# Optimization experiments

Measured on AMD Instinct MI355X. Metric: run time of the kernel, lower is better.

Reference implementation:

```python
import jax, jax.numpy as jnp
import numpy as np

N_REGS, R_BIT, N_OPS, FLIP = 8, 16, 16, 2

def bit2dec(bits):
    # little-endian soft bits -> decimal: sum_k b_k * 2^k
    k = jnp.arange(bits.shape[-1], dtype=bits.dtype)
    return jnp.sum(bits * jnp.exp2(k), axis=-1)

def addr_w(idx, n):
    # differentiable soft one-hot over n slots (linear interpolation kernel)
    grid = jnp.arange(n, dtype=idx.dtype)
    return jnp.maximum(1.0 - jnp.abs(idx[..., None] - grid), 0.0)

def setup_inputs():
    key = jax.random.key(0)
    ks = jax.random.split(key, 12)
    B, H, I, L = 8192, 512, 1024, 16
    return dict(
        z_hidden=jax.random.normal(ks[0], (B, H), jnp.float32),
        P_op=jax.random.uniform(ks[1], (B, L, 4), dtype=jnp.float32),
        P_dst=jax.random.uniform(ks[2], (B, L, 3), dtype=jnp.float32),
        P_src1=jax.random.uniform(ks[3], (B, L, 3), dtype=jnp.float32),
        P_src2=jax.random.uniform(ks[4], (B, L, 3), dtype=jnp.float32),
        P_imm=jax.random.uniform(ks[5], (B, L, 3), dtype=jnp.float32),
        Proglen=jax.random.uniform(ks[6], (B, 4), dtype=jnp.float32),
        group_num=16,
        W1=jax.random.normal(ks[7], (H, I), jnp.float32) / np.sqrt(H).astype(np.float32),
        b1=jnp.zeros((I,), jnp.float32),
        WR=jax.random.normal(ks[8], (I, N_REGS * R_BIT), jnp.float32) / np.sqrt(I).astype(np.float32),
        bR=jnp.zeros((N_REGS * R_BIT,), jnp.float32),
        Wt=jax.random.normal(ks[9], (I, 1), jnp.float32) / np.sqrt(I).astype(np.float32),
        bt=jnp.zeros((1,), jnp.float32),
        W_r2h=jax.random.normal(ks[10], (N_REGS, H), jnp.float32) / np.sqrt(N_REGS).astype(np.float32),
        b_r2h=jnp.zeros((H,), jnp.float32),
        ln_g=jnp.ones((H,), jnp.float32),
        ln_b=jnp.zeros((H,), jnp.float32),
    )

def reference(z_hidden, P_op, P_dst, P_src1, P_src2, P_imm, Proglen, group_num,
              W1, b1, WR, bR, Wt, bt, W_r2h, b_r2h, ln_g, ln_b):
    B, L, G = z_hidden.shape[0], P_op.shape[1], group_num
    # ---- Augmentation_Layer: MLP head -> R soft-bits + threshold ----
    h = jax.nn.relu(z_hidden @ W1 + b1)
    R_bits = jax.nn.sigmoid(h @ WR + bR).reshape(B, N_REGS, R_BIT)
    threshold = jax.nn.sigmoid(h @ Wt + bt)                 # [B,1]
    # ---- GroupSample.generate4R: flip FLIP random R-bits per candidate (cand 0 = original) ----
    idx = jax.random.randint(jax.random.key(42), (B, G, FLIP), 0, N_REGS * R_BIT)
    mask = jnp.clip(jax.nn.one_hot(idx, N_REGS * R_BIT, dtype=jnp.float32).sum(-2), 0.0, 1.0)
    mask = mask.at[:, 0].set(0.0).reshape(B, G, N_REGS, R_BIT)
    Rb = R_bits[:, None]                                    # [B,1,n_regs,r_bit]
    R = bit2dec(Rb + mask * (1.0 - 2.0 * Rb))               # [B,G,n_regs] decimals
    M = jnp.zeros_like(R)
    prog_len = jnp.broadcast_to(bit2dec(Proglen)[:, None], (B, G))
    dec = lambda x: bit2dec(x).T                            # [L,B]
    prog = (dec(P_op), dec(P_dst), dec(P_src1), dec(P_src2), dec(P_imm),
            jnp.arange(L, dtype=jnp.float32))

    # ---- MultiInterpreter: differentiable soft register machine ----
    def step(carry, xs):
        R, M = carry
        op_t, dst_t, s1_t, s2_t, imm_t, t = xs
        bc = lambda v: jnp.broadcast_to(v[:, None], (B, G))
        op_t, dst_t, s1_t, s2_t, imm_t = map(bc, (op_t, dst_t, s1_t, s2_t, imm_t))
        active = jnp.clip(prog_len - t, 0.0, 1.0)           # halt mask [B,G]
        w_d = addr_w(dst_t, N_REGS)                         # [B,G,n_regs]
        w_1 = addr_w(s1_t, N_REGS)
        w_2 = addr_w(s2_t, N_REGS)
        w_op = addr_w(op_t, N_OPS)                          # [B,G,16]
        r1 = jnp.sum(w_1 * R, -1); r2 = jnp.sum(w_2 * R, -1)
        m1 = jnp.sum(w_1 * M, -1); old = jnp.sum(w_d * R, -1)
        results = jnp.stack([
            old,                       # 0 NOP
            r1 + r2,                   # 1 ADD
            r1 - r2,                   # 2 SUB
            r1 * r2 / 65536.0,         # 3 MUL (scaled by 2^r_bit)
            r1,                        # 4 MOV
            imm_t,                     # 5 LOADI
            r1 + imm_t,                # 6 ADDI
            jnp.maximum(r1, r2),       # 7 MAX
            jnp.minimum(r1, r2),       # 8 MIN
            -r1,                       # 9 NEG
            0.5 * r1,                  # 10 SHR
            r2,                        # 11 MOV2
            m1,                        # 12 LOAD M[src1]
            old,                       # 13 STORE (reg unchanged)
            jnp.abs(r1),               # 14 ABS
            old,                       # 15 NOP
        ], axis=-1)
        res = jnp.sum(w_op * results, -1)                   # [B,G]
        p_store = w_op[..., 13]
        R = R + active[..., None] * w_d * (res[..., None] - R)
        M = M + (active * p_store)[..., None] * w_d * (r1[..., None] - M)
        return (R, M), None

    (R, M), _ = jax.lax.scan(step, (R, M), prog)
    # ---- register2hidden + LayerNorm ----
    reg_hidden = R @ W_r2h + b_r2h                          # [B,G,H]
    mu = reg_hidden.mean(-1, keepdims=True)
    var = reg_hidden.var(-1, keepdims=True)
    reg_hidden = (reg_hidden - mu) * jax.lax.rsqrt(var + 1e-5) * ln_g + ln_b
    return reg_hidden, threshold
```

## Files before the change

### kernel.cpp

```cpp
#include <hip/hip_runtime.h>
#include <stdint.h>

typedef __attribute__((ext_vector_type(8))) short short8;
typedef __attribute__((ext_vector_type(4))) float f32x4;
typedef __attribute__((ext_vector_type(8))) unsigned short ushort8;
typedef __attribute__((ext_vector_type(4))) unsigned short ushort4v;

__device__ __forceinline__ unsigned short f2bf(float f) {
  uint32_t u = __float_as_uint(f);
  uint32_t r = (u + 0x7fffu + ((u >> 16) & 1u)) >> 16;
  return (unsigned short)r;
}
__device__ __forceinline__ float bf2f(unsigned short v) {
  return __uint_as_float(((uint32_t)v) << 16);
}

__device__ __forceinline__ uint32_t rotl32(uint32_t v, int d) { return (v << d) | (v >> (32 - d)); }

__device__ __forceinline__ void threefry2x32(uint32_t k0, uint32_t k1, uint32_t& x0, uint32_t& x1) {
  const uint32_t ks2 = k0 ^ k1 ^ 0x1BD11BDAu;
  x0 += k0; x1 += k1;
  x0 += x1; x1 = rotl32(x1, 13); x1 ^= x0;
  x0 += x1; x1 = rotl32(x1, 15); x1 ^= x0;
  x0 += x1; x1 = rotl32(x1, 26); x1 ^= x0;
  x0 += x1; x1 = rotl32(x1, 6);  x1 ^= x0;
  x0 += k1; x1 += ks2 + 1u;
  x0 += x1; x1 = rotl32(x1, 17); x1 ^= x0;
  x0 += x1; x1 = rotl32(x1, 29); x1 ^= x0;
  x0 += x1; x1 = rotl32(x1, 16); x1 ^= x0;
  x0 += x1; x1 = rotl32(x1, 24); x1 ^= x0;
  x0 += ks2; x1 += k0 + 2u;
  x0 += x1; x1 = rotl32(x1, 13); x1 ^= x0;
  x0 += x1; x1 = rotl32(x1, 15); x1 ^= x0;
  x0 += x1; x1 = rotl32(x1, 26); x1 ^= x0;
  x0 += x1; x1 = rotl32(x1, 6);  x1 ^= x0;
  x0 += k0; x1 += k1 + 3u;
  x0 += x1; x1 = rotl32(x1, 17); x1 ^= x0;
  x0 += x1; x1 = rotl32(x1, 29); x1 ^= x0;
  x0 += x1; x1 = rotl32(x1, 16); x1 ^= x0;
  x0 += x1; x1 = rotl32(x1, 24); x1 ^= x0;
  x0 += k1; x1 += ks2 + 4u;
  x0 += x1; x1 = rotl32(x1, 13); x1 ^= x0;
  x0 += x1; x1 = rotl32(x1, 15); x1 ^= x0;
  x0 += x1; x1 = rotl32(x1, 26); x1 ^= x0;
  x0 += x1; x1 = rotl32(x1, 6);  x1 ^= x0;
  x0 += ks2; x1 += k0 + 5u;
}

__global__ __launch_bounds__(256) void cast_bf16(const float* __restrict__ in,
                                                 unsigned short* __restrict__ o, int n8) {
  const int i = blockIdx.x * 256 + threadIdx.x;
  if (i >= n8) return;
  const float4 a = reinterpret_cast<const float4*>(in)[i * 2];
  const float4 b = reinterpret_cast<const float4*>(in)[i * 2 + 1];
  ushort8 u;
  u[0] = f2bf(a.x); u[1] = f2bf(a.y); u[2] = f2bf(a.z); u[3] = f2bf(a.w);
  u[4] = f2bf(b.x); u[5] = f2bf(b.y); u[6] = f2bf(b.z); u[7] = f2bf(b.w);
  reinterpret_cast<ushort8*>(o)[i] = u;
}

__global__ __launch_bounds__(256) void transpose_cast(const float* __restrict__ W1,
                                                      const float* __restrict__ WR,
                                                      unsigned short* __restrict__ W1t,
                                                      unsigned short* __restrict__ WRt) {
  __shared__ float t[32][33];
  const int tid = threadIdx.x;
  const float* src; unsigned short* dst; int N, K, k0, n0;
  if (blockIdx.x < 512) {
    src = W1; dst = W1t; N = 1024; K = 512;
    k0 = (blockIdx.x & 15) * 32; n0 = (blockIdx.x >> 4) * 32;
  } else {
    const int b2 = blockIdx.x - 512;
    src = WR; dst = WRt; N = 128; K = 1024;
    k0 = (b2 & 31) * 32; n0 = (b2 >> 5) * 32;
  }
  {
    const int row = tid >> 3, c4 = (tid & 7) * 4;
    const float4 v = *reinterpret_cast<const float4*>(&src[(size_t)(k0 + row) * N + n0 + c4]);
    t[row][c4] = v.x; t[row][c4 + 1] = v.y; t[row][c4 + 2] = v.z; t[row][c4 + 3] = v.w;
  }
  __syncthreads();
  {
    const int n = tid >> 3, k4 = (tid & 7) * 4;
    ushort4v o;
    o.x = f2bf(t[k4 + 0][n]); o.y = f2bf(t[k4 + 1][n]);
    o.z = f2bf(t[k4 + 2][n]); o.w = f2bf(t[k4 + 3][n]);
    *reinterpret_cast<ushort4v*>(&dst[(size_t)(n0 + n) * K + k0 + k4]) = o;
  }
}

__global__ __launch_bounds__(256) void gemm_fused(const unsigned short* __restrict__ zb,
                                                  const unsigned short* __restrict__ W1t,
                                                  const float* __restrict__ b1,
                                                  const unsigned short* __restrict__ WRt,
                                                  unsigned short* __restrict__ h,
                                                  float* __restrict__ part, int B) {
  __shared__ __align__(16) char smem[34816];
  auto As = reinterpret_cast<unsigned short (*)[56]>(smem);
  auto Bs = reinterpret_cast<unsigned short (*)[56]>(smem + 14336);
  auto H2 = reinterpret_cast<unsigned short (*)[136]>(smem);

  const int tid = threadIdx.x;
  const int lane = tid & 63, wave = tid >> 6;
  const int wm = wave >> 1, wn = wave & 1;
  const int bx = blockIdx.x, bm = blockIdx.y * 128, bn = bx * 128;

  f32x4 acc[4][4];
#pragma unroll
  for (int i = 0; i < 4; ++i)
#pragma unroll
    for (int j = 0; j < 4; ++j) acc[i][j] = (f32x4)0.f;

  const int sm = tid >> 1, skh = (tid & 1) * 16;
  const int fr = lane & 15, kc = (lane >> 4) * 8;
  const int lr = (lane >> 4) * 4, lc = lane & 15;

  for (int k0 = 0; k0 < 512; k0 += 32) {
    {
      const unsigned short* ap = &zb[(size_t)(bm + sm) * 512 + k0 + skh];
      *reinterpret_cast<ushort8*>(&As[sm][skh]) = *reinterpret_cast<const ushort8*>(ap);
      *reinterpret_cast<ushort8*>(&As[sm][skh + 8]) = *reinterpret_cast<const ushort8*>(ap + 8);
    }
    {
      const unsigned short* bp = &W1t[(size_t)(bn + sm) * 512 + k0 + skh];
      *reinterpret_cast<ushort8*>(&Bs[sm][skh]) = *reinterpret_cast<const ushort8*>(bp);
      *reinterpret_cast<ushort8*>(&Bs[sm][skh + 8]) = *reinterpret_cast<const ushort8*>(bp + 8);
    }
    __syncthreads();
    short8 af[4], bfv[4];
#pragma unroll
    for (int f = 0; f < 4; ++f)
      af[f] = *reinterpret_cast<const short8*>(&As[wm * 64 + f * 16 + fr][kc]);
#pragma unroll
    for (int f = 0; f < 4; ++f)
      bfv[f] = *reinterpret_cast<const short8*>(&Bs[wn * 64 + f * 16 + fr][kc]);
#pragma unroll
    for (int fm = 0; fm < 4; ++fm)
#pragma unroll
      for (int fn = 0; fn < 4; ++fn)
        acc[fm][fn] = __builtin_amdgcn_mfma_f32_16x16x32_bf16(af[fm], bfv[fn], acc[fm][fn], 0, 0, 0);
    __syncthreads();
  }

#pragma unroll
  for (int fn = 0; fn < 4; ++fn) {
    const int col_l = wn * 64 + fn * 16 + lc;
    const float bv = b1[bn + col_l];
#pragma unroll
    for (int fm = 0; fm < 4; ++fm) {
      const int row_l0 = wm * 64 + fm * 16 + lr;
#pragma unroll
      for (int r = 0; r < 4; ++r)
        H2[row_l0 + r][col_l] = f2bf(fmaxf(acc[fm][fn][r] + bv, 0.f));
    }
  }
  __syncthreads();

  {
    const int row = tid >> 1, c0 = (tid & 1) * 64;
    unsigned short* hp = &h[(size_t)(bm + row) * 1024 + bn + c0];
#pragma unroll
    for (int j = 0; j < 8; ++j)
      *reinterpret_cast<ushort8*>(hp + j * 8) = *reinterpret_cast<const ushort8*>(&H2[row][c0 + j * 8]);
  }

  f32x4 acc2[4][4];
#pragma unroll
  for (int i = 0; i < 4; ++i)
#pragma unroll
    for (int j = 0; j < 4; ++j) acc2[i][j] = (f32x4)0.f;

#pragma unroll
  for (int ks = 0; ks < 4; ++ks) {
    short8 af2[4], bf2v[4];
#pragma unroll
    for (int fm = 0; fm < 4; ++fm)
      af2[fm] = *reinterpret_cast<const short8*>(&H2[wm * 64 + fm * 16 + fr][ks * 32 + kc]);
#pragma unroll
    for (int fn = 0; fn < 4; ++fn)
      bf2v[fn] = *reinterpret_cast<const short8*>(
          &WRt[(size_t)(wn * 64 + fn * 16 + fr) * 1024 + bn + ks * 32 + kc]);
#pragma unroll
    for (int fm = 0; fm < 4; ++fm)
#pragma unroll
      for (int fn = 0; fn < 4; ++fn)
        acc2[fm][fn] = __builtin_amdgcn_mfma_f32_16x16x32_bf16(af2[fm], bf2v[fn], acc2[fm][fn], 0, 0, 0);
  }

  float* pp = part + (size_t)bx * B * 128;
#pragma unroll
  for (int fn = 0; fn < 4; ++fn) {
    const int col = wn * 64 + fn * 16 + lc;
#pragma unroll
    for (int fm = 0; fm < 4; ++fm) {
      const int row0 = bm + wm * 64 + fm * 16 + lr;
#pragma unroll
      for (int r = 0; r < 4; ++r)
        pp[(size_t)(row0 + r) * 128 + col] = acc2[fm][fn][r];
    }
  }
}

__global__ __launch_bounds__(256) void reduce_sig(const float* __restrict__ part,
                                                  const float* __restrict__ bR,
                                                  float* __restrict__ out, int total4) {
  const int i = blockIdx.x * 256 + threadIdx.x;
  if (i >= total4) return;
  const float4* p = reinterpret_cast<const float4*>(part);
  float4 s = p[i];
#pragma unroll
  for (int j = 1; j < 8; ++j) {
    const float4 q = p[i + (size_t)j * total4];
    s.x += q.x; s.y += q.y; s.z += q.z; s.w += q.w;
  }
  const int col = (i * 4) & 127;
  const float4 bb = *reinterpret_cast<const float4*>(&bR[col]);
  float4 o;
  o.x = 1.f / (1.f + expf(-(s.x + bb.x)));
  o.y = 1.f / (1.f + expf(-(s.y + bb.y)));
  o.z = 1.f / (1.f + expf(-(s.z + bb.z)));
  o.w = 1.f / (1.f + expf(-(s.w + bb.w)));
  reinterpret_cast<float4*>(out)[i] = o;
}

__global__ __launch_bounds__(256) void thresh_kernel(const unsigned short* __restrict__ h,
                                                     const float* __restrict__ Wt,
                                                     const float* __restrict__ bt,
                                                     float* __restrict__ out, int B) {
  const int lane = threadIdx.x & 63;
  const int row = blockIdx.x * 4 + (threadIdx.x >> 6);
  if (row >= B) return;
  const unsigned short* hr = h + (size_t)row * 1024;
  float s = 0.f;
#pragma unroll
  for (int it = 0; it < 2; ++it) {
    const int k = (lane + it * 64) * 8;
    const ushort8 a = *reinterpret_cast<const ushort8*>(&hr[k]);
    const float4 w0 = *reinterpret_cast<const float4*>(&Wt[k]);
    const float4 w1 = *reinterpret_cast<const float4*>(&Wt[k + 4]);
    s += bf2f(a[0]) * w0.x + bf2f(a[1]) * w0.y + bf2f(a[2]) * w0.z + bf2f(a[3]) * w0.w;
    s += bf2f(a[4]) * w1.x + bf2f(a[5]) * w1.y + bf2f(a[6]) * w1.z + bf2f(a[7]) * w1.w;
  }
#pragma unroll
  for (int off = 32; off; off >>= 1) s += __shfl_xor(s, off);
  if (lane == 0) out[row] = 1.f / (1.f + expf(-(s + bt[0])));
}

__global__ __launch_bounds__(256) void decode_prog(const float* __restrict__ P_op,
                                                   const float* __restrict__ P_dst,
                                                   const float* __restrict__ P_s1,
                                                   const float* __restrict__ P_s2,
                                                   const float* __restrict__ P_imm,
                                                   const float* __restrict__ Plen,
                                                   float* __restrict__ prog,
                                                   float* __restrict__ plen, int BT) {
  const int i = blockIdx.x * 256 + threadIdx.x;
  if (i >= BT) return;
  const float* po = P_op + (size_t)i * 4;
  const float op = po[0] + 2.f * po[1] + 4.f * po[2] + 8.f * po[3];
  const float* pd = P_dst + (size_t)i * 3;
  const float dv = pd[0] + 2.f * pd[1] + 4.f * pd[2];
  const float* p1 = P_s1 + (size_t)i * 3;
  const float s1v = p1[0] + 2.f * p1[1] + 4.f * p1[2];
  const float* p2 = P_s2 + (size_t)i * 3;
  const float s2v = p2[0] + 2.f * p2[1] + 4.f * p2[2];
  const float* pi = P_imm + (size_t)i * 3;
  const float imv = pi[0] + 2.f * pi[1] + 4.f * pi[2];
  float* o = prog + (size_t)i * 5;
  o[0] = op; o[1] = dv; o[2] = s1v; o[3] = s2v; o[4] = imv;
  if ((i & 15) == 0) {
    const int b = i >> 4;
    const float* pl = Plen + (size_t)b * 4;
    plen[b] = pl[0] + 2.f * pl[1] + 4.f * pl[2] + 8.f * pl[3];
  }
}

__global__ __launch_bounds__(256) void scan_kernel(const float* __restrict__ Rbits,
                                                   const float* __restrict__ prog,
                                                   const float* __restrict__ plen,
                                                   float* __restrict__ Rfinal, int B) {
  __shared__ float s_bits[16][128];
  __shared__ float s_prog[16][80];
  __shared__ float s_plen[16];
  const int tid = threadIdx.x;
  const int b0 = blockIdx.x * 16;
#pragma unroll
  for (int j = 0; j < 8; ++j) {
    const int f = tid + 256 * j;
    s_bits[f >> 7][f & 127] = Rbits[(size_t)(b0 + (f >> 7)) * 128 + (f & 127)];
  }
#pragma unroll
  for (int j = 0; j < 5; ++j) {
    const int f = tid + 256 * j;
    s_prog[f / 80][f % 80] = prog[(size_t)b0 * 80 + f];
  }
  if (tid < 16) s_plen[tid] = plen[b0 + tid];
  __syncthreads();

  const int lb = tid >> 4, g = tid & 15;
  const int bg = (b0 + lb) * 16 + g;

  uint32_t k2a, k2b;
  { uint32_t x0 = 0u, x1 = 1u; threefry2x32(0u, 42u, x0, x1); k2a = x0; k2b = x1; }
  uint32_t p0, p1;
  {
    uint32_t x0 = 0u, x1 = (uint32_t)bg * 2u;
    threefry2x32(k2a, k2b, x0, x1);
    p0 = (x0 ^ x1) & 127u;
  }
  {
    uint32_t x0 = 0u, x1 = (uint32_t)bg * 2u + 1u;
    threefry2x32(k2a, k2b, x0, x1);
    p1 = (x0 ^ x1) & 127u;
  }

  float R[8], M[8];
#pragma unroll
  for (int r = 0; r < 8; ++r) {
    float a = 0.f;
#pragma unroll
    for (int bit = 0; bit < 16; ++bit) {
      const int pos = r * 16 + bit;
      float v = s_bits[lb][pos];
      const bool flip = (g != 0) && ((int)p0 == pos || (int)p1 == pos);
      v = flip ? 1.0f - v : v;
      a = fmaf(v, (float)(1 << bit), a);
    }
    R[r] = a;
    M[r] = 0.f;
  }

  const float pl = s_plen[lb];
  for (int t = 0; t < 16; ++t) {
    const float op = s_prog[lb][t * 5 + 0];
    const float dst = s_prog[lb][t * 5 + 1];
    const float sa = s_prog[lb][t * 5 + 2];
    const float sb = s_prog[lb][t * 5 + 3];
    const float imm = s_prog[lb][t * 5 + 4];
    const float active = fminf(fmaxf(pl - (float)t, 0.f), 1.f);
    float r1 = 0.f, r2 = 0.f, m1 = 0.f, old = 0.f;
    float wd[8];
#pragma unroll
    for (int i = 0; i < 8; ++i) {
      const float w1 = fmaxf(1.f - fabsf(sa - (float)i), 0.f);
      const float w2 = fmaxf(1.f - fabsf(sb - (float)i), 0.f);
      wd[i] = fmaxf(1.f - fabsf(dst - (float)i), 0.f);
      r1 = fmaf(w1, R[i], r1);
      r2 = fmaf(w2, R[i], r2);
      m1 = fmaf(w1, M[i], m1);
      old = fmaf(wd[i], R[i], old);
    }
    float results[16];
    results[0] = old;               results[1] = r1 + r2;
    results[2] = r1 - r2;           results[3] = r1 * r2 * (1.f / 65536.f);
    results[4] = r1;                results[5] = imm;
    results[6] = r1 + imm;          results[7] = fmaxf(r1, r2);
    results[8] = fminf(r1, r2);     results[9] = -r1;
    results[10] = 0.5f * r1;        results[11] = r2;
    results[12] = m1;               results[13] = old;
    results[14] = fabsf(r1);        results[15] = old;
    float res = 0.f;
    const float pstore = fmaxf(1.f - fabsf(op - 13.f), 0.f);
#pragma unroll
    for (int o = 0; o < 16; ++o) res = fmaf(fmaxf(1.f - fabsf(op - (float)o), 0.f), results[o], res);
#pragma unroll
    for (int i = 0; i < 8; ++i) {
      R[i] = fmaf(active * wd[i], res - R[i], R[i]);
      M[i] = fmaf(active * pstore * wd[i], r1 - M[i], M[i]);
    }
  }

  float* outp = Rfinal + (size_t)bg * 8;
#pragma unroll
  for (int r = 0; r < 8; ++r) outp[r] = R[r];
}

__global__ __launch_bounds__(256) void final_expand2(const float* __restrict__ Rf,
                                                     const float* __restrict__ W,
                                                     const float* __restrict__ bias,
                                                     const float* __restrict__ gam,
                                                     const float* __restrict__ bet,
                                                     float* __restrict__ out, int rowsPerWave) {
  const int lane = threadIdx.x & 63;
  const int w = blockIdx.x * 4 + (threadIdx.x >> 6);
  const int h0 = lane * 8;

  float wreg[8][8];
#pragma unroll
  for (int reg = 0; reg < 8; ++reg) {
    const float4 wa = *reinterpret_cast<const float4*>(&W[reg * 512 + h0]);
    const float4 wb = *reinterpret_cast<const float4*>(&W[reg * 512 + h0 + 4]);
    wreg[reg][0] = wa.x; wreg[reg][1] = wa.y; wreg[reg][2] = wa.z; wreg[reg][3] = wa.w;
    wreg[reg][4] = wb.x; wreg[reg][5] = wb.y; wreg[reg][6] = wb.z; wreg[reg][7] = wb.w;
  }
  float bi[8], ga[8], be[8];
  {
    const float4 a = *reinterpret_cast<const float4*>(&bias[h0]);
    const float4 b = *reinterpret_cast<const float4*>(&bias[h0 + 4]);
    bi[0] = a.x; bi[1] = a.y; bi[2] = a.z; bi[3] = a.w; bi[4] = b.x; bi[5] = b.y; bi[6] = b.z; bi[7] = b.w;
    const float4 c = *reinterpret_cast<const float4*>(&gam[h0]);
    const float4 d = *reinterpret_cast<const float4*>(&gam[h0 + 4]);
    ga[0] = c.x; ga[1] = c.y; ga[2] = c.z; ga[3] = c.w; ga[4] = d.x; ga[5] = d.y; ga[6] = d.z; ga[7] = d.w;
    const float4 e = *reinterpret_cast<const float4*>(&bet[h0]);
    const float4 f = *reinterpret_cast<const float4*>(&bet[h0 + 4]);
    be[0] = e.x; be[1] = e.y; be[2] = e.z; be[3] = e.w; be[4] = f.x; be[5] = f.y; be[6] = f.z; be[7] = f.w;
  }

  const int r0 = w * rowsPerWave;
  for (int i = 0; i < rowsPerWave; ++i) {
    const int row = r0 + i;
    const float4 ra = *reinterpret_cast<const float4*>(&Rf[(size_t)row * 8]);
    const float4 rb = *reinterpret_cast<const float4*>(&Rf[(size_t)row * 8 + 4]);
    const float r[8] = {ra.x, ra.y, ra.z, ra.w, rb.x, rb.y, rb.z, rb.w};
    float x[8];
#pragma unroll
    for (int j = 0; j < 8; ++j) x[j] = bi[j];
#pragma unroll
    for (int reg = 0; reg < 8; ++reg)
#pragma unroll
      for (int j = 0; j < 8; ++j) x[j] = fmaf(r[reg], wreg[reg][j], x[j]);
    float s1 = 0.f, s2 = 0.f;
#pragma unroll
    for (int j = 0; j < 8; ++j) { s1 += x[j]; s2 = fmaf(x[j], x[j], s2); }
#pragma unroll
    for (int off = 32; off; off >>= 1) { s1 += __shfl_xor(s1, off); s2 += __shfl_xor(s2, off); }
    const float mean = s1 * (1.f / 512.f);
    const float var = s2 * (1.f / 512.f) - mean * mean;
    const float inv = rsqrtf(var + 1e-5f);
    float y[8];
#pragma unroll
    for (int j = 0; j < 8; ++j) y[j] = (x[j] - mean) * inv * ga[j] + be[j];
    float* dst = out + (size_t)row * 512 + h0;
    *reinterpret_cast<float4*>(dst) = make_float4(y[0], y[1], y[2], y[3]);
    *reinterpret_cast<float4*>(dst + 4) = make_float4(y[4], y[5], y[6], y[7]);
  }
}

extern "C" void kernel_launch(void* const* d_in, const int* in_sizes, int n_in,
                              void* d_out, int out_size, void* d_ws, size_t ws_size,
                              hipStream_t stream) {
  const float* z    = (const float*)d_in[0];
  const float* P_op = (const float*)d_in[1];
  const float* P_dst= (const float*)d_in[2];
  const float* P_s1 = (const float*)d_in[3];
  const float* P_s2 = (const float*)d_in[4];
  const float* P_imm= (const float*)d_in[5];
  const float* Plen = (const float*)d_in[6];
  const float* W1   = (const float*)d_in[8];
  const float* b1   = (const float*)d_in[9];
  const float* WR   = (const float*)d_in[10];
  const float* bR   = (const float*)d_in[11];
  const float* Wt   = (const float*)d_in[12];
  const float* bt   = (const float*)d_in[13];
  const float* W_r2h= (const float*)d_in[14];
  const float* b_r2h= (const float*)d_in[15];
  const float* ln_g = (const float*)d_in[16];
  const float* ln_b = (const float*)d_in[17];

  const int B = in_sizes[0] / 512;
  float* out = (float*)d_out;
  unsigned short* h = (unsigned short*)out;
  float* part    = out + (size_t)(1 << 25);
  float* thr_out = out + (size_t)B * 16 * 512;

  float* ws = (float*)d_ws;
  float* Rbits  = ws;
  float* prog   = Rbits + (size_t)B * 128;
  float* plen   = prog + (size_t)B * 80;
  float* Rfinal = plen + B;
  unsigned short* W1t = (unsigned short*)(Rfinal + (size_t)B * 128);
  unsigned short* WRt = W1t + (size_t)1024 * 512;
  unsigned short* zb  = WRt + (size_t)128 * 1024;

  const dim3 blk(256);
  cast_bf16<<<dim3(B * 512 / 8 / 256), blk, 0, stream>>>(z, zb, B * 512 / 8);
  transpose_cast<<<dim3(640), blk, 0, stream>>>(W1, WR, W1t, WRt);
  gemm_fused<<<dim3(8, B / 128), blk, 0, stream>>>(zb, W1t, b1, WRt, h, part, B);
  reduce_sig<<<dim3((B * 128 / 4 + 255) / 256), blk, 0, stream>>>(part, bR, Rbits, B * 128 / 4);
  thresh_kernel<<<dim3(B / 4), blk, 0, stream>>>(h, Wt, bt, thr_out, B);
  decode_prog<<<dim3((B * 16 + 255) / 256), blk, 0, stream>>>(P_op, P_dst, P_s1, P_s2, P_imm,
                                                              Plen, prog, plen, B * 16);
  scan_kernel<<<dim3(B / 16), blk, 0, stream>>>(Rbits, prog, plen, Rfinal, B);
  final_expand2<<<dim3(B * 16 / 4 / 32), blk, 0, stream>>>(Rfinal, W_r2h, b_r2h, ln_g, ln_b, out,
                                                           32);
}
```

Before: 129.0 us.

## Merge prep kernels, fold split-K reduce into scan, deepen GEMM K-tile

Casting z, transposing the weights and decoding the program now run as one launch with block-index dispatch. The split-K partial reduction and sigmoid are folded into the scan kernel's shared-memory load, which removes the reduce_sig launch and the Rbits round trip through global memory. The first GEMM's K tile grows from 32 to 64 with a wider padded LDS row, so there are half as many barriers per tile. The cost is a little more shared memory and longer per-thread load loops.

```diff
diff --git a/kernel.cpp b/kernel.cpp
--- a/kernel.cpp
+++ b/kernel.cpp
@@ -47,45 +47,76 @@
   x0 += ks2; x1 += k0 + 5u;
 }
 
-__global__ __launch_bounds__(256) void cast_bf16(const float* __restrict__ in,
-                                                 unsigned short* __restrict__ o, int n8) {
-  const int i = blockIdx.x * 256 + threadIdx.x;
-  if (i >= n8) return;
-  const float4 a = reinterpret_cast<const float4*>(in)[i * 2];
-  const float4 b = reinterpret_cast<const float4*>(in)[i * 2 + 1];
-  ushort8 u;
-  u[0] = f2bf(a.x); u[1] = f2bf(a.y); u[2] = f2bf(a.z); u[3] = f2bf(a.w);
-  u[4] = f2bf(b.x); u[5] = f2bf(b.y); u[6] = f2bf(b.z); u[7] = f2bf(b.w);
-  reinterpret_cast<ushort8*>(o)[i] = u;
-}
-
-__global__ __launch_bounds__(256) void transpose_cast(const float* __restrict__ W1,
-                                                      const float* __restrict__ WR,
-                                                      unsigned short* __restrict__ W1t,
-                                                      unsigned short* __restrict__ WRt) {
+__global__ __launch_bounds__(256) void prep_kernel(const float* __restrict__ z,
+                                                   unsigned short* __restrict__ zb, int n8,
+                                                   const float* __restrict__ W1,
+                                                   const float* __restrict__ WR,
+                                                   unsigned short* __restrict__ W1t,
+                                                   unsigned short* __restrict__ WRt,
+                                                   const float* __restrict__ P_op,
+                                                   const float* __restrict__ P_dst,
+                                                   const float* __restrict__ P_s1,
+                                                   const float* __restrict__ P_s2,
+                                                   const float* __restrict__ P_imm,
+                                                   const float* __restrict__ Plen,
+                                                   float* __restrict__ prog,
+                                                   float* __restrict__ plen, int BT) {
   __shared__ float t[32][33];
   const int tid = threadIdx.x;
-  const float* src; unsigned short* dst; int N, K, k0, n0;
-  if (blockIdx.x < 512) {
-    src = W1; dst = W1t; N = 1024; K = 512;
-    k0 = (blockIdx.x & 15) * 32; n0 = (blockIdx.x >> 4) * 32;
+  const int bx = blockIdx.x;
+  if (bx < 2048) {
+    const int i = bx * 256 + tid;
+    if (i >= n8) return;
+    const float4 a = reinterpret_cast<const float4*>(z)[i * 2];
+    const float4 b = reinterpret_cast<const float4*>(z)[i * 2 + 1];
+    ushort8 u;
+    u[0] = f2bf(a.x); u[1] = f2bf(a.y); u[2] = f2bf(a.z); u[3] = f2bf(a.w);
+    u[4] = f2bf(b.x); u[5] = f2bf(b.y); u[6] = f2bf(b.z); u[7] = f2bf(b.w);
+    reinterpret_cast<ushort8*>(zb)[i] = u;
+  } else if (bx < 2688) {
+    const int b = bx - 2048;
+    const float* src; unsigned short* dst; int N, K, k0, n0;
+    if (b < 512) {
+      src = W1; dst = W1t; N = 1024; K = 512;
+      k0 = (b & 15) * 32; n0 = (b >> 4) * 32;
+    } else {
+      const int b2 = b - 512;
+      src = WR; dst = WRt; N = 128; K = 1024;
+      k0 = (b2 & 31) * 32; n0 = (b2 >> 5) * 32;
+    }
+    {
+      const int row = tid >> 3, c4 = (tid & 7) * 4;
+      const float4 v = *reinterpret_cast<const float4*>(&src[(size_t)(k0 + row) * N + n0 + c4]);
+      t[row][c4] = v.x; t[row][c4 + 1] = v.y; t[row][c4 + 2] = v.z; t[row][c4 + 3] = v.w;
+    }
+    __syncthreads();
+    {
+      const int n = tid >> 3, k4 = (tid & 7) * 4;
+      ushort4v o;
+      o.x = f2bf(t[k4 + 0][n]); o.y = f2bf(t[k4 + 1][n]);
+      o.z = f2bf(t[k4 + 2][n]); o.w = f2bf(t[k4 + 3][n]);
+      *reinterpret_cast<ushort4v*>(&dst[(size_t)(n0 + n) * K + k0 + k4]) = o;
+    }
   } else {
-    const int b2 = blockIdx.x - 512;
-    src = WR; dst = WRt; N = 128; K = 1024;
-    k0 = (b2 & 31) * 32; n0 = (b2 >> 5) * 32;
-  }
-  {
-    const int row = tid >> 3, c4 = (tid & 7) * 4;
-    const float4 v = *reinterpret_cast<const float4*>(&src[(size_t)(k0 + row) * N + n0 + c4]);
-    t[row][c4] = v.x; t[row][c4 + 1] = v.y; t[row][c4 + 2] = v.z; t[row][c4 + 3] = v.w;
-  }
-  __syncthreads();
-  {
-    const int n = tid >> 3, k4 = (tid & 7) * 4;
-    ushort4v o;
-    o.x = f2bf(t[k4 + 0][n]); o.y = f2bf(t[k4 + 1][n]);
-    o.z = f2bf(t[k4 + 2][n]); o.w = f2bf(t[k4 + 3][n]);
-    *reinterpret_cast<ushort4v*>(&dst[(size_t)(n0 + n) * K + k0 + k4]) = o;
+    const int i = (bx - 2688) * 256 + tid;
+    if (i >= BT) return;
+    const float* po = P_op + (size_t)i * 4;
+    const float op = po[0] + 2.f * po[1] + 4.f * po[2] + 8.f * po[3];
+    const float* pd = P_dst + (size_t)i * 3;
+    const float dv = pd[0] + 2.f * pd[1] + 4.f * pd[2];
+    const float* p1 = P_s1 + (size_t)i * 3;
+    const float s1v = p1[0] + 2.f * p1[1] + 4.f * p1[2];
+    const float* p2 = P_s2 + (size_t)i * 3;
+    const float s2v = p2[0] + 2.f * p2[1] + 4.f * p2[2];
+    const float* pi = P_imm + (size_t)i * 3;
+    const float imv = pi[0] + 2.f * pi[1] + 4.f * pi[2];
+    float* o = prog + (size_t)i * 5;
+    o[0] = op; o[1] = dv; o[2] = s1v; o[3] = s2v; o[4] = imv;
+    if ((i & 15) == 0) {
+      const int b = i >> 4;
+      const float* pl = Plen + (size_t)b * 4;
+      plen[b] = pl[0] + 2.f * pl[1] + 4.f * pl[2] + 8.f * pl[3];
+    }
   }
 }
 
@@ -95,9 +126,9 @@
                                                   const unsigned short* __restrict__ WRt,
                                                   unsigned short* __restrict__ h,
                                                   float* __restrict__ part, int B) {
-  __shared__ __align__(16) char smem[34816];
-  auto As = reinterpret_cast<unsigned short (*)[56]>(smem);
-  auto Bs = reinterpret_cast<unsigned short (*)[56]>(smem + 14336);
+  __shared__ __align__(16) char smem[36864];
+  auto As = reinterpret_cast<unsigned short (*)[72]>(smem);
+  auto Bs = reinterpret_cast<unsigned short (*)[72]>(smem + 18432);
   auto H2 = reinterpret_cast<unsigned short (*)[136]>(smem);
 
   const int tid = threadIdx.x;
@@ -111,34 +142,41 @@
 #pragma unroll
     for (int j = 0; j < 4; ++j) acc[i][j] = (f32x4)0.f;
 
-  const int sm = tid >> 1, skh = (tid & 1) * 16;
+  const int sm = tid >> 1, skb = (tid & 1) * 32;
   const int fr = lane & 15, kc = (lane >> 4) * 8;
   const int lr = (lane >> 4) * 4, lc = lane & 15;
 
-  for (int k0 = 0; k0 < 512; k0 += 32) {
+  for (int k0 = 0; k0 < 512; k0 += 64) {
     {
-      const unsigned short* ap = &zb[(size_t)(bm + sm) * 512 + k0 + skh];
-      *reinterpret_cast<ushort8*>(&As[sm][skh]) = *reinterpret_cast<const ushort8*>(ap);
-      *reinterpret_cast<ushort8*>(&As[sm][skh + 8]) = *reinterpret_cast<const ushort8*>(ap + 8);
+      const unsigned short* ap = &zb[(size_t)(bm + sm) * 512 + k0 + skb];
+#pragma unroll
+      for (int j = 0; j < 4; ++j)
+        *reinterpret_cast<ushort8*>(&As[sm][skb + j * 8]) =
+            *reinterpret_cast<const ushort8*>(ap + j * 8);
     }
     {
-      const unsigned short* bp = &W1t[(size_t)(bn + sm) * 512 + k0 + skh];
-      *reinterpret_cast<ushort8*>(&Bs[sm][skh]) = *reinterpret_cast<const ushort8*>(bp);
-      *reinterpret_cast<ushort8*>(&Bs[sm][skh + 8]) = *reinterpret_cast<const ushort8*>(bp + 8);
+      const unsigned short* bp = &W1t[(size_t)(bn + sm) * 512 + k0 + skb];
+#pragma unroll
+      for (int j = 0; j < 4; ++j)
+        *reinterpret_cast<ushort8*>(&Bs[sm][skb + j * 8]) =
+            *reinterpret_cast<const ushort8*>(bp + j * 8);
     }
     __syncthreads();
-    short8 af[4], bfv[4];
-#pragma unroll
-    for (int f = 0; f < 4; ++f)
-      af[f] = *reinterpret_cast<const short8*>(&As[wm * 64 + f * 16 + fr][kc]);
-#pragma unroll
-    for (int f = 0; f < 4; ++f)
-      bfv[f] = *reinterpret_cast<const short8*>(&Bs[wn * 64 + f * 16 + fr][kc]);
-#pragma unroll
-    for (int fm = 0; fm < 4; ++fm)
-#pragma unroll
-      for (int fn = 0; fn < 4; ++fn)
-        acc[fm][fn] = __builtin_amdgcn_mfma_f32_16x16x32_bf16(af[fm], bfv[fn], acc[fm][fn], 0, 0, 0);
+#pragma unroll
+    for (int s = 0; s < 2; ++s) {
+      short8 af[4], bfv[4];
+#pragma unroll
+      for (int f = 0; f < 4; ++f)
+        af[f] = *reinterpret_cast<const short8*>(&As[wm * 64 + f * 16 + fr][s * 32 + kc]);
+#pragma unroll
+      for (int f = 0; f < 4; ++f)
+        bfv[f] = *reinterpret_cast<const short8*>(&Bs[wn * 64 + f * 16 + fr][s * 32 + kc]);
+#pragma unroll
+      for (int fm = 0; fm < 4; ++fm)
+#pragma unroll
+        for (int fn = 0; fn < 4; ++fn)
+          acc[fm][fn] = __builtin_amdgcn_mfma_f32_16x16x32_bf16(af[fm], bfv[fn], acc[fm][fn], 0, 0, 0);
+    }
     __syncthreads();
   }
 
@@ -199,28 +237,6 @@
         pp[(size_t)(row0 + r) * 128 + col] = acc2[fm][fn][r];
     }
   }
-}
-
-__global__ __launch_bounds__(256) void reduce_sig(const float* __restrict__ part,
-                                                  const float* __restrict__ bR,
-                                                  float* __restrict__ out, int total4) {
-  const int i = blockIdx.x * 256 + threadIdx.x;
-  if (i >= total4) return;
-  const float4* p = reinterpret_cast<const float4*>(part);
-  float4 s = p[i];
-#pragma unroll
-  for (int j = 1; j < 8; ++j) {
-    const float4 q = p[i + (size_t)j * total4];
-    s.x += q.x; s.y += q.y; s.z += q.z; s.w += q.w;
-  }
-  const int col = (i * 4) & 127;
-  const float4 bb = *reinterpret_cast<const float4*>(&bR[col]);
-  float4 o;
-  o.x = 1.f / (1.f + expf(-(s.x + bb.x)));
-  o.y = 1.f / (1.f + expf(-(s.y + bb.y)));
-  o.z = 1.f / (1.f + expf(-(s.z + bb.z)));
-  o.w = 1.f / (1.f + expf(-(s.w + bb.w)));
-  reinterpret_cast<float4*>(out)[i] = o;
 }
 
 __global__ __launch_bounds__(256) void thresh_kernel(const unsigned short* __restrict__ h,
@@ -246,39 +262,11 @@
   if (lane == 0) out[row] = 1.f / (1.f + expf(-(s + bt[0])));
 }
 
-__global__ __launch_bounds__(256) void decode_prog(const float* __restrict__ P_op,
-                                                   const float* __restrict__ P_dst,
-                                                   const float* __restrict__ P_s1,
-                                                   const float* __restrict__ P_s2,
-                                                   const float* __restrict__ P_imm,
-                                                   const float* __restrict__ Plen,
-                                                   float* __restrict__ prog,
-                                                   float* __restrict__ plen, int BT) {
-  const int i = blockIdx.x * 256 + threadIdx.x;
-  if (i >= BT) return;
-  const float* po = P_op + (size_t)i * 4;
-  const float op = po[0] + 2.f * po[1] + 4.f * po[2] + 8.f * po[3];
-  const float* pd = P_dst + (size_t)i * 3;
-  const float dv = pd[0] + 2.f * pd[1] + 4.f * pd[2];
-  const float* p1 = P_s1 + (size_t)i * 3;
-  const float s1v = p1[0] + 2.f * p1[1] + 4.f * p1[2];
-  const float* p2 = P_s2 + (size_t)i * 3;
-  const float s2v = p2[0] + 2.f * p2[1] + 4.f * p2[2];
-  const float* pi = P_imm + (size_t)i * 3;
-  const float imv = pi[0] + 2.f * pi[1] + 4.f * pi[2];
-  float* o = prog + (size_t)i * 5;
-  o[0] = op; o[1] = dv; o[2] = s1v; o[3] = s2v; o[4] = imv;
-  if ((i & 15) == 0) {
-    const int b = i >> 4;
-    const float* pl = Plen + (size_t)b * 4;
-    plen[b] = pl[0] + 2.f * pl[1] + 4.f * pl[2] + 8.f * pl[3];
-  }
-}
-
-__global__ __launch_bounds__(256) void scan_kernel(const float* __restrict__ Rbits,
-                                                   const float* __restrict__ prog,
-                                                   const float* __restrict__ plen,
-                                                   float* __restrict__ Rfinal, int B) {
+__global__ __launch_bounds__(256) void scan2_kernel(const float* __restrict__ part,
+                                                    const float* __restrict__ bR,
+                                                    const float* __restrict__ prog,
+                                                    const float* __restrict__ plen,
+                                                    float* __restrict__ Rfinal, int B) {
   __shared__ float s_bits[16][128];
   __shared__ float s_prog[16][80];
   __shared__ float s_plen[16];
@@ -287,7 +275,12 @@
 #pragma unroll
   for (int j = 0; j < 8; ++j) {
     const int f = tid + 256 * j;
-    s_bits[f >> 7][f & 127] = Rbits[(size_t)(b0 + (f >> 7)) * 128 + (f & 127)];
+    const int lb = f >> 7, c = f & 127;
+    float s = part[(size_t)(b0 + lb) * 128 + c];
+#pragma unroll
+    for (int sl = 1; sl < 8; ++sl)
+      s += part[(size_t)sl * B * 128 + (size_t)(b0 + lb) * 128 + c];
+    s_bits[lb][c] = 1.f / (1.f + expf(-(s + bR[c])));
   }
 #pragma unroll
   for (int j = 0; j < 5; ++j) {
@@ -464,8 +457,7 @@
   float* thr_out = out + (size_t)B * 16 * 512;
 
   float* ws = (float*)d_ws;
-  float* Rbits  = ws;
-  float* prog   = Rbits + (size_t)B * 128;
+  float* prog   = ws;
   float* plen   = prog + (size_t)B * 80;
   float* Rfinal = plen + B;
   unsigned short* W1t = (unsigned short*)(Rfinal + (size_t)B * 128);
@@ -473,14 +465,12 @@
   unsigned short* zb  = WRt + (size_t)128 * 1024;
 
   const dim3 blk(256);
-  cast_bf16<<<dim3(B * 512 / 8 / 256), blk, 0, stream>>>(z, zb, B * 512 / 8);
-  transpose_cast<<<dim3(640), blk, 0, stream>>>(W1, WR, W1t, WRt);
+  prep_kernel<<<dim3(3200), blk, 0, stream>>>(z, zb, B * 512 / 8, W1, WR, W1t, WRt,
+                                              P_op, P_dst, P_s1, P_s2, P_imm, Plen,
+                                              prog, plen, B * 16);
   gemm_fused<<<dim3(8, B / 128), blk, 0, stream>>>(zb, W1t, b1, WRt, h, part, B);
-  reduce_sig<<<dim3((B * 128 / 4 + 255) / 256), blk, 0, stream>>>(part, bR, Rbits, B * 128 / 4);
   thresh_kernel<<<dim3(B / 4), blk, 0, stream>>>(h, Wt, bt, thr_out, B);
-  decode_prog<<<dim3((B * 16 + 255) / 256), blk, 0, stream>>>(P_op, P_dst, P_s1, P_s2, P_imm,
-                                                              Plen, prog, plen, B * 16);
-  scan_kernel<<<dim3(B / 16), blk, 0, stream>>>(Rbits, prog, plen, Rfinal, B);
+  scan2_kernel<<<dim3(B / 16), blk, 0, stream>>>(part, bR, prog, plen, Rfinal, B);
   final_expand2<<<dim3(B * 16 / 4 / 32), blk, 0, stream>>>(Rfinal, W_r2h, b_r2h, ln_g, ln_b, out,
                                                            32);
 }
```

New measurement: 120.9 us. 6.2% less time.
